# Performance work log

Hardware: AMD Instinct MI355X
Metric: run time of the kernel (lower is better)

## Reference

```python
import jax, jax.numpy as jnp
import numpy as np

N_NODES = 100000
N_EDGES = 1600000
T = 24
F_IN = 16
H = 128
OUT = 64


def setup_inputs() -> dict:
    key = jax.random.key(0)
    ks = jax.random.split(key, 12)
    s = 0.05
    return {
        "x_time_series": jax.random.normal(ks[0], (N_NODES, T, F_IN), jnp.float32),
        "edge_index": jax.random.randint(ks[1], (2, N_EDGES), 0, N_NODES, jnp.int64),
        "gru_W_ih": jax.random.normal(ks[2], (3 * H, F_IN), jnp.float32) * s,
        "gru_W_hh": jax.random.normal(ks[3], (3 * H, H), jnp.float32) * s,
        "gru_b_ih": jax.random.normal(ks[4], (3 * H,), jnp.float32) * s,
        "gru_b_hh": jax.random.normal(ks[5], (3 * H,), jnp.float32) * s,
        "lin1_l_W": jax.random.normal(ks[6], (H, H), jnp.float32) * s,
        "lin1_l_b": jax.random.normal(ks[7], (H,), jnp.float32) * s,
        "lin1_r_W": jax.random.normal(ks[8], (H, H), jnp.float32) * s,
        "lin2_l_W": jax.random.normal(ks[9], (OUT, H), jnp.float32) * s,
        "lin2_l_b": jax.random.normal(ks[10], (OUT,), jnp.float32) * s,
        "lin2_r_W": jax.random.normal(ks[11], (OUT, H), jnp.float32) * s,
    }


def gru_last(x, W_ih, W_hh, b_ih, b_hh):
    # x: [N, T, F]; single-layer batch_first GRU, return last hidden state [N, H]
    Hd = W_hh.shape[1]
    # precompute input projections for all steps: [T, N, 3H]
    gi_all = jnp.einsum('ntf,gf->tng', x, W_ih) + b_ih

    def step(h, gi):
        gh = h @ W_hh.T + b_hh
        r = jax.nn.sigmoid(gi[:, :Hd] + gh[:, :Hd])
        z = jax.nn.sigmoid(gi[:, Hd:2 * Hd] + gh[:, Hd:2 * Hd])
        n = jnp.tanh(gi[:, 2 * Hd:] + r * gh[:, 2 * Hd:])
        h_new = (1.0 - z) * n + z * h
        return h_new, None

    h0 = jnp.zeros((x.shape[0], Hd), x.dtype)
    h_last, _ = jax.lax.scan(step, h0, gi_all)
    return h_last


def sage_conv(x, edge_index, W_l, b_l, W_r):
    # PyG SAGEConv with mean aggregation:
    #   out_i = W_l @ mean_{j->i} x_j + b_l + W_r @ x_i
    src, dst = edge_index[0], edge_index[1]
    n = x.shape[0]
    msg = x[src]                                   # [E, F] irregular gather
    agg = jax.ops.segment_sum(msg, dst, num_segments=n)
    cnt = jax.ops.segment_sum(jnp.ones((msg.shape[0],), x.dtype), dst, num_segments=n)
    mean = agg / jnp.maximum(cnt, 1.0)[:, None]
    return mean @ W_l.T + b_l + x @ W_r.T


def reference(x_time_series, edge_index, gru_W_ih, gru_W_hh, gru_b_ih, gru_b_hh,
              lin1_l_W, lin1_l_b, lin1_r_W, lin2_l_W, lin2_l_b, lin2_r_W):
    x = x_time_series.reshape(-1, T, F_IN)
    h = gru_last(x, gru_W_ih, gru_W_hh, gru_b_ih, gru_b_hh)   # [N, H]
    g = sage_conv(h, edge_index, lin1_l_W, lin1_l_b, lin1_r_W) + h
    g = jax.nn.relu(g)
    # dropout in eval mode -> identity
    out = sage_conv(g, edge_index, lin2_l_W, lin2_l_b, lin2_r_W)
    return out
```

## Files before the change

### kernel.cpp

```cpp
#include <hip/hip_runtime.h>
#include <math.h>

#define NND 100000
#define TT 24
#define FI 16
#define HD 128
#define GD 384
#define OD 64
#define NE 1600000

typedef __bf16 bf16x8 __attribute__((ext_vector_type(8)));
typedef float f32x4 __attribute__((ext_vector_type(4)));
typedef unsigned short u16;
typedef unsigned int u32;

#define S_RZ (-1.44269504f)
#define S_N  (-2.88539008f)

__device__ __forceinline__ u16 f2b(float f) {
    u32 u = __float_as_uint(f);
    u32 r = (u + 0x7FFFu + ((u >> 16) & 1u)) >> 16;
    return (u16)r;
}
__device__ __forceinline__ u32 cvtpk(float lo, float hi) {
    u32 r;
    asm("v_cvt_pk_bf16_f32 %0, %1, %2" : "=v"(r) : "v"(lo), "v"(hi));
    return r;
}
__device__ __forceinline__ float b2f(u16 v) {
    return __uint_as_float((u32)v << 16);
}

__global__ void cvt_x_kernel(const float* __restrict__ x, u16* __restrict__ xb) {
    size_t base = ((size_t)blockIdx.x * 256 + threadIdx.x) * 8;
    float4 a = *(const float4*)(x + base);
    float4 b = *(const float4*)(x + base + 4);
    u32 o0 = cvtpk(a.x, a.y), o1 = cvtpk(a.z, a.w);
    u32 o2 = cvtpk(b.x, b.y), o3 = cvtpk(b.z, b.w);
    *(uint4*)(xb + base) = make_uint4(o0, o1, o2, o3);
}

__global__ void pack_w_kernel(const float* __restrict__ Whh, const float* __restrict__ Wih,
                              const float* __restrict__ bih, const float* __restrict__ bhh,
                              u16* __restrict__ Ap, u16* __restrict__ Aip) {
    int id = blockIdx.x * 256 + threadIdx.x;
    if (id < 6144) {
        int lane = id & 63, fs = id >> 6;
        int s = fs & 3, gt = fs >> 2;
        int row = gt * 16 + (lane & 15);
        float sc = (row < 2 * HD) ? S_RZ : S_N;
        int k0 = s * 32 + (lane >> 4) * 8;
        const float* src = Whh + (size_t)row * HD + k0;
        u16 o[8];
#pragma unroll
        for (int e = 0; e < 8; ++e) o[e] = f2b(src[e] * sc);
        u32* dst = (u32*)(Ap + (size_t)id * 8);
#pragma unroll
        for (int e = 0; e < 4; ++e) dst[e] = (u32)o[2 * e] | ((u32)o[2 * e + 1] << 16);
    } else if (id < 7680) {
        int id2 = id - 6144;
        int lane = id2 & 63, gt = id2 >> 6;
        int row = gt * 16 + (lane & 15);
        float sc = (row < 2 * HD) ? S_RZ : S_N;
        int g = lane >> 4;
        u16 o[8] = {0, 0, 0, 0, 0, 0, 0, 0};
        if (g < 2) {
            const float* src = Wih + (size_t)row * FI + g * 8;
#pragma unroll
            for (int e = 0; e < 8; ++e) o[e] = f2b(src[e] * sc);
        } else if (g == 2) {
            float bias = (row < 2 * HD) ? (bih[row] + bhh[row]) : bih[row];
            o[0] = f2b(bias * sc);
        }
        u32* dst = (u32*)(Aip + (size_t)id2 * 8);
#pragma unroll
        for (int e = 0; e < 4; ++e) dst[e] = (u32)o[2 * e] | ((u32)o[2 * e + 1] << 16);
    }
}

__global__ void pack_gemm_kernel(const float* __restrict__ W, u16* __restrict__ F, int rows) {
    int id = blockIdx.x * 256 + threadIdx.x;
    if (id >= rows * 16) return;
    int lane = id & 63, fs = id >> 6;
    int s = fs & 3, tile = fs >> 2;
    int row = tile * 16 + (lane & 15);
    int k0 = s * 32 + (lane >> 4) * 8;
    const float* src = W + (size_t)row * HD + k0;
    u16 o[8];
#pragma unroll
    for (int e = 0; e < 8; ++e) o[e] = f2b(src[e]);
    u32* dst = (u32*)(F + (size_t)id * 8);
#pragma unroll
    for (int e = 0; e < 4; ++e) dst[e] = (u32)o[2 * e] | ((u32)o[2 * e + 1] << 16);
}

__device__ __forceinline__ int hidx(int row, int col) {
    return row * 128 + (col ^ ((row & 7) << 3));
}

__global__ __launch_bounds__(512) void gru_mfma_kernel(
    const u16* __restrict__ xb,
    const u16* __restrict__ Ap,
    const u16* __restrict__ Aip,
    const float* __restrict__ bhh,
    float* __restrict__ hout,
    u16* __restrict__ h16)
{
    __shared__ u16 hb0[64 * 128];
    __shared__ u16 hb1[64 * 128];

    const int tid = threadIdx.x;
    const int w = tid >> 6, lane = tid & 63;
    const int l15 = lane & 15, g = lane >> 4;
    const int gbase = blockIdx.x * 64;
    const int j0 = w * 16 + g * 4;

    for (int i = tid; i < 64 * 128 / 2; i += 512) ((u32*)hb0)[i] = 0u;

    bf16x8 Ah[3][4], Ai[3];
#pragma unroll
    for (int a = 0; a < 3; ++a) {
        int gt = w + a * 8;
#pragma unroll
        for (int s = 0; s < 4; ++s)
            Ah[a][s] = *(const bf16x8*)(Ap + ((size_t)(gt * 4 + s) * 64 + lane) * 8);
        Ai[a] = *(const bf16x8*)(Aip + ((size_t)gt * 64 + lane) * 8);
    }

    f32x4 bnh4 = *(const f32x4*)(bhh + 256 + j0);
#pragma unroll
    for (int r = 0; r < 4; ++r) bnh4[r] *= S_N;

    const f32x4 fz = {0.f, 0.f, 0.f, 0.f};
    bf16x8 xdef;
    {
        uint4 u = make_uint4(0u, 0u, 0u, 0u);
        if (g == 2) u.x = 0x3F80u;
        *(uint4*)&xdef = u;
    }

    f32x4 hreg[4];
#pragma unroll
    for (int m = 0; m < 4; ++m) hreg[m] = fz;

    int xoff[4];
#pragma unroll
    for (int m = 0; m < 4; ++m) {
        int nd = gbase + m * 16 + l15;
        nd = nd < NND ? nd : NND - 1;
        xoff[m] = nd * (TT * FI) + g * 8;
    }

    __syncthreads();

    auto dostep = [&](int t, const u16* __restrict__ rb, u16* __restrict__ wb) {
#pragma unroll
        for (int mh = 0; mh < 2; ++mh) {
            const int ma = mh * 2, mb = mh * 2 + 1;
            bf16x8 xf0 = xdef, xf1 = xdef;
            if (g < 2) {
                xf0 = *(const bf16x8*)(xb + (size_t)(xoff[ma] + t * FI));
                xf1 = *(const bf16x8*)(xb + (size_t)(xoff[mb] + t * FI));
            }

            const int ra = ma * 16 + l15, rbr = mb * 16 + l15;
            bf16x8 b0[4], b1[4];
#pragma unroll
            for (int s = 0; s < 4; ++s) {
                b0[s] = *(const bf16x8*)&rb[hidx(ra, s * 32 + g * 8)];
                b1[s] = *(const bf16x8*)&rb[hidx(rbr, s * 32 + g * 8)];
            }

            f32x4 acc[3][2], acci[2];
#pragma unroll
            for (int a = 0; a < 3; ++a) {
                acc[a][0] = __builtin_amdgcn_mfma_f32_16x16x32_bf16(Ah[a][0], b0[0], fz, 0, 0, 0);
                acc[a][1] = __builtin_amdgcn_mfma_f32_16x16x32_bf16(Ah[a][0], b1[0], fz, 0, 0, 0);
            }
#pragma unroll
            for (int s = 1; s < 4; ++s) {
#pragma unroll
                for (int a = 0; a < 3; ++a) {
                    acc[a][0] = __builtin_amdgcn_mfma_f32_16x16x32_bf16(Ah[a][s], b0[s], acc[a][0], 0, 0, 0);
                    acc[a][1] = __builtin_amdgcn_mfma_f32_16x16x32_bf16(Ah[a][s], b1[s], acc[a][1], 0, 0, 0);
                }
            }
            acc[0][0] = __builtin_amdgcn_mfma_f32_16x16x32_bf16(Ai[0], xf0, acc[0][0], 0, 0, 0);
            acc[1][0] = __builtin_amdgcn_mfma_f32_16x16x32_bf16(Ai[1], xf0, acc[1][0], 0, 0, 0);
            acci[0]   = __builtin_amdgcn_mfma_f32_16x16x32_bf16(Ai[2], xf0, fz, 0, 0, 0);
            acc[0][1] = __builtin_amdgcn_mfma_f32_16x16x32_bf16(Ai[0], xf1, acc[0][1], 0, 0, 0);
            acc[1][1] = __builtin_amdgcn_mfma_f32_16x16x32_bf16(Ai[1], xf1, acc[1][1], 0, 0, 0);
            acci[1]   = __builtin_amdgcn_mfma_f32_16x16x32_bf16(Ai[2], xf1, fz, 0, 0, 0);

#pragma unroll
            for (int mi = 0; mi < 2; ++mi) {
                int m = mh * 2 + mi;
#pragma unroll
                for (int r = 0; r < 4; ++r) {
                    float rr = __builtin_amdgcn_rcpf(1.0f + __builtin_amdgcn_exp2f(acc[0][mi][r]));
                    float zz = __builtin_amdgcn_rcpf(1.0f + __builtin_amdgcn_exp2f(acc[1][mi][r]));
                    float na = acci[mi][r] + rr * (acc[2][mi][r] + bnh4[r]);
                    float nn = 2.0f * __builtin_amdgcn_rcpf(1.0f + __builtin_amdgcn_exp2f(na)) - 1.0f;
                    float h = nn + zz * (hreg[m][r] - nn);
                    hreg[m][r] = h;
                }
                u32 p0 = cvtpk(hreg[m][0], hreg[m][1]);
                u32 p1 = cvtpk(hreg[m][2], hreg[m][3]);
                *(uint2*)&wb[hidx(m * 16 + l15, j0)] = make_uint2(p0, p1);
            }
        }
        __syncthreads();
    };

#pragma unroll 1
    for (int tt = 0; tt < TT; tt += 2) {
        dostep(tt, hb0, hb1);
        dostep(tt + 1, hb1, hb0);
    }

#pragma unroll
    for (int m = 0; m < 4; ++m) {
        int nd = gbase + m * 16 + l15;
        if (nd < NND) {
            *(f32x4*)(hout + (size_t)nd * HD + j0) = hreg[m];
            u32 c0 = cvtpk(hreg[m][0], hreg[m][1]);
            u32 c1 = cvtpk(hreg[m][2], hreg[m][3]);
            *(uint2*)(h16 + (size_t)nd * HD + j0) = make_uint2(c0, c1);
        }
    }
}

template <int M, bool RES>
__global__ __launch_bounds__(512) void proj2_mfma_kernel(
    const u16* __restrict__ X16,
    const u16* __restrict__ Wl,
    const u16* __restrict__ Wr,
    const float* __restrict__ bias,
    const float* __restrict__ Xres,
    u16* __restrict__ P16,
    float* __restrict__ Q)
{
    __shared__ u16 xs[64 * 128];

    const int tid = threadIdx.x;
    const int w = tid >> 6, lane = tid & 63;
    const int l15 = lane & 15, g = lane >> 4;
    const int gbase = blockIdx.x * 64;
    const f32x4 fz = {0.f, 0.f, 0.f, 0.f};

#pragma unroll
    for (int i = 0; i < 2; ++i) {
        int lin = tid + 512 * i;
        int n = lin >> 4;
        int k8 = (lin & 15) * 8;
        int gn = gbase + n; if (gn >= NND) gn = NND - 1;
        uint4 v = *(const uint4*)(X16 + (size_t)gn * HD + k8);
        *(uint4*)&xs[hidx(n, k8)] = v;
    }
    __syncthreads();

    if constexpr (M == 128) {
        bf16x8 Al[4], Ar[4];
#pragma unroll
        for (int s = 0; s < 4; ++s) {
            Al[s] = *(const bf16x8*)(Wl + ((size_t)(w * 4 + s) * 64 + lane) * 8);
            Ar[s] = *(const bf16x8*)(Wr + ((size_t)(w * 4 + s) * 64 + lane) * 8);
        }
        const int f0 = w * 16 + g * 4;
        f32x4 bq = *(const f32x4*)(bias + f0);

#pragma unroll
        for (int m = 0; m < 4; ++m) {
            bf16x8 b[4];
#pragma unroll
            for (int s = 0; s < 4; ++s)
                b[s] = *(const bf16x8*)&xs[hidx(m * 16 + l15, s * 32 + g * 8)];
            f32x4 ap = fz, aq = fz;
#pragma unroll
            for (int s = 0; s < 4; ++s) {
                ap = __builtin_amdgcn_mfma_f32_16x16x32_bf16(Al[s], b[s], ap, 0, 0, 0);
                aq = __builtin_amdgcn_mfma_f32_16x16x32_bf16(Ar[s], b[s], aq, 0, 0, 0);
            }
            int nd = gbase + m * 16 + l15;
            if (nd < NND) {
                u32 c0 = cvtpk(ap[0], ap[1]), c1 = cvtpk(ap[2], ap[3]);
                *(uint2*)(P16 + (size_t)nd * M + f0) = make_uint2(c0, c1);
                f32x4 v = aq + bq;
                if constexpr (RES) v += *(const f32x4*)(Xres + (size_t)nd * HD + f0);
                *(f32x4*)(Q + (size_t)nd * M + f0) = v;
            }
        }
    } else {
        const int tile = w & 3;
        const bool isQ = (w >= 4);
        const u16* Wsel = isQ ? Wr : Wl;
        bf16x8 A[4];
#pragma unroll
        for (int s = 0; s < 4; ++s)
            A[s] = *(const bf16x8*)(Wsel + ((size_t)(tile * 4 + s) * 64 + lane) * 8);
        const int f0 = tile * 16 + g * 4;
        f32x4 bq = *(const f32x4*)(bias + f0);

#pragma unroll
        for (int m = 0; m < 4; ++m) {
            bf16x8 b[4];
#pragma unroll
            for (int s = 0; s < 4; ++s)
                b[s] = *(const bf16x8*)&xs[hidx(m * 16 + l15, s * 32 + g * 8)];
            f32x4 a = fz;
#pragma unroll
            for (int s = 0; s < 4; ++s)
                a = __builtin_amdgcn_mfma_f32_16x16x32_bf16(A[s], b[s], a, 0, 0, 0);
            int nd = gbase + m * 16 + l15;
            if (nd < NND) {
                if (isQ) {
                    f32x4 v = a + bq;
                    *(f32x4*)(Q + (size_t)nd * M + f0) = v;
                } else {
                    u32 c0 = cvtpk(a[0], a[1]), c1 = cvtpk(a[2], a[3]);
                    *(uint2*)(P16 + (size_t)nd * M + f0) = make_uint2(c0, c1);
                }
            }
        }
    }
}

__global__ void count_kernel(const int* __restrict__ dst, int* __restrict__ cnt) {
    int e = blockIdx.x * 256 + threadIdx.x;
    if (e < NE) atomicAdd(&cnt[dst[e]], 1);
}

__global__ void blocksum_kernel(const int* __restrict__ cnt, int* __restrict__ bsum) {
    __shared__ int sh[256];
    int b = blockIdx.x, t = threadIdx.x;
    int base = b * 1024;
    int s = 0;
    for (int i = t; i < 1024; i += 256) {
        int idx = base + i;
        s += (idx < NND) ? cnt[idx] : 0;
    }
    sh[t] = s; __syncthreads();
    for (int o = 128; o > 0; o >>= 1) { if (t < o) sh[t] += sh[t + o]; __syncthreads(); }
    if (t == 0) bsum[b] = sh[0];
}

__global__ void scanbsum_kernel(int* __restrict__ bsum, int nb, int* __restrict__ rowptr) {
    if (threadIdx.x == 0 && blockIdx.x == 0) {
        int acc = 0;
        for (int i = 0; i < nb; ++i) { int v = bsum[i]; bsum[i] = acc; acc += v; }
        rowptr[NND] = NE;
    }
}

__global__ void scan_kernel(const int* __restrict__ cnt, const int* __restrict__ bsum,
                            int* __restrict__ rowptr) {
    __shared__ int sh[256];
    int b = blockIdx.x, t = threadIdx.x;
    int base = b * 1024;
    int v[4], loc = 0;
#pragma unroll
    for (int j = 0; j < 4; ++j) {
        int idx = base + t * 4 + j;
        v[j] = (idx < NND) ? cnt[idx] : 0;
        loc += v[j];
    }
    sh[t] = loc; __syncthreads();
    for (int o = 1; o < 256; o <<= 1) {
        int x = (t >= o) ? sh[t - o] : 0;
        __syncthreads();
        sh[t] += x;
        __syncthreads();
    }
    int acc = bsum[b] + sh[t] - loc;
#pragma unroll
    for (int j = 0; j < 4; ++j) {
        int idx = base + t * 4 + j;
        if (idx < NND) rowptr[idx] = acc;
        acc += v[j];
    }
}

__global__ void fill_kernel(const int* __restrict__ src, const int* __restrict__ dst,
                            const int* __restrict__ rowptr, int* __restrict__ fill,
                            int* __restrict__ csr) {
    int e = blockIdx.x * 256 + threadIdx.x;
    if (e >= NE) return;
    int d = dst[e];
    int pos = rowptr[d] + atomicAdd(&fill[d], 1);
    csr[pos] = src[e];
}

__global__ __launch_bounds__(256) void gather1_kernel(
    const u16* __restrict__ P16,
    const int* __restrict__ rowptr, const int* __restrict__ csr,
    const float* __restrict__ q,
    u16* __restrict__ g16)
{
    int n = ((blockIdx.x * 256 + threadIdx.x) >> 6);
    if (n >= NND) return;
    int lane = threadIdx.x & 63;
    int beg = rowptr[n], end = rowptr[n + 1];

    float ax = 0.f, ay = 0.f;
    for (int cb = beg; cb < end; cb += 64) {
        int myi = (cb + lane < end) ? csr[cb + lane] : 0;
        int nn = min(end - cb, 64);
        for (int i = 0; i < nn; ++i) {
            int s = __shfl(myi, i);
            u32 pv = *(const u32*)(P16 + (size_t)s * HD + lane * 2);
            ax += b2f((u16)pv); ay += b2f((u16)(pv >> 16));
        }
    }
    int deg = end - beg;
    float inv = 1.0f / (float)(deg > 0 ? deg : 1);
    float2 qv = *(const float2*)(q + (size_t)n * HD + lane * 2);
    float r0 = fmaxf(ax * inv + qv.x, 0.f);
    float r1 = fmaxf(ay * inv + qv.y, 0.f);
    *(u32*)(g16 + (size_t)n * HD + lane * 2) = cvtpk(r0, r1);
}

__global__ __launch_bounds__(256) void gather2_kernel(
    const u16* __restrict__ P16,
    const int* __restrict__ rowptr, const int* __restrict__ csr,
    const float* __restrict__ q,
    float* __restrict__ outp)
{
    int n = ((blockIdx.x * 256 + threadIdx.x) >> 6);
    if (n >= NND) return;
    int lane = threadIdx.x & 63;
    int beg = rowptr[n], end = rowptr[n + 1];

    float a = 0.f;
    for (int cb = beg; cb < end; cb += 64) {
        int myi = (cb + lane < end) ? csr[cb + lane] : 0;
        int nn = min(end - cb, 64);
        for (int i = 0; i < nn; ++i) {
            int s = __shfl(myi, i);
            a += b2f(P16[(size_t)s * OD + lane]);
        }
    }
    int deg = end - beg;
    float inv = 1.0f / (float)(deg > 0 ? deg : 1);
    outp[(size_t)n * OD + lane] = a * inv + q[(size_t)n * OD + lane];
}

extern "C" void kernel_launch(void* const* d_in, const int* in_sizes, int n_in,
                              void* d_out, int out_size, void* d_ws, size_t ws_size,
                              hipStream_t stream) {
    const float* x   = (const float*)d_in[0];
    const int*   edg = (const int*)d_in[1];
    const int*   src = edg;
    const int*   dst = edg + NE;
    const float* Wih = (const float*)d_in[2];
    const float* Whh = (const float*)d_in[3];
    const float* bih = (const float*)d_in[4];
    const float* bhh = (const float*)d_in[5];
    const float* W1l = (const float*)d_in[6];
    const float* b1  = (const float*)d_in[7];
    const float* W1r = (const float*)d_in[8];
    const float* W2l = (const float*)d_in[9];
    const float* b2  = (const float*)d_in[10];
    const float* W2r = (const float*)d_in[11];
    float* out = (float*)d_out;

    char* wsp = (char*)d_ws;
    auto alloc = [&](size_t nbytes) {
        char* p = wsp; wsp += (nbytes + 255) & ~(size_t)255; return p;
    };
    u16*   Ap    = (u16*)alloc((size_t)6144 * 8 * 2);
    u16*   Aip   = (u16*)alloc((size_t)1536 * 8 * 2);
    u16*   Pw1l  = (u16*)alloc((size_t)2048 * 8 * 2);
    u16*   Pw1r  = (u16*)alloc((size_t)2048 * 8 * 2);
    u16*   Pw2l  = (u16*)alloc((size_t)1024 * 8 * 2);
    u16*   Pw2r  = (u16*)alloc((size_t)1024 * 8 * 2);
    int*   cnt   = (int*)alloc((size_t)NND * 4);
    int*   fill  = (int*)alloc((size_t)NND * 4);
    int*   rowp  = (int*)alloc((size_t)(NND + 1) * 4);
    int*   bsum  = (int*)alloc((size_t)128 * 4);
    int*   csr   = (int*)alloc((size_t)NE * 4);
    float* h     = (float*)alloc((size_t)NND * HD * 4);
    u16*   h16   = (u16*)alloc((size_t)NND * HD * 2);
    float* q     = (float*)alloc((size_t)NND * HD * 4);
    u16*   P16   = (u16*)alloc((size_t)NND * HD * 2);
    u16*   g16   = (u16*)alloc((size_t)NND * HD * 2);
    u16*   xb    = (u16*)q;
    float* q2    = q;
    u16*   P16b  = P16;

    const int NB_SCAN = (NND + 1023) / 1024;

    hipMemsetAsync(cnt, 0, (size_t)NND * 4, stream);
    hipMemsetAsync(fill, 0, (size_t)NND * 4, stream);

    cvt_x_kernel<<<(NND * TT * FI) / (256 * 8), 256, 0, stream>>>(x, xb);
    pack_w_kernel<<<30, 256, 0, stream>>>(Whh, Wih, bih, bhh, Ap, Aip);
    pack_gemm_kernel<<<8, 256, 0, stream>>>(W1l, Pw1l, HD);
    pack_gemm_kernel<<<8, 256, 0, stream>>>(W1r, Pw1r, HD);
    pack_gemm_kernel<<<4, 256, 0, stream>>>(W2l, Pw2l, OD);
    pack_gemm_kernel<<<4, 256, 0, stream>>>(W2r, Pw2r, OD);

    count_kernel<<<(NE + 255) / 256, 256, 0, stream>>>(dst, cnt);
    blocksum_kernel<<<NB_SCAN, 256, 0, stream>>>(cnt, bsum);
    scanbsum_kernel<<<1, 64, 0, stream>>>(bsum, NB_SCAN, rowp);
    scan_kernel<<<NB_SCAN, 256, 0, stream>>>(cnt, bsum, rowp);
    fill_kernel<<<(NE + 255) / 256, 256, 0, stream>>>(src, dst, rowp, fill, csr);

    const int nblk = (NND + 63) / 64;
    gru_mfma_kernel<<<nblk, 512, 0, stream>>>(xb, Ap, Aip, bhh, h, h16);

    proj2_mfma_kernel<HD, true><<<nblk, 512, 0, stream>>>(h16, Pw1l, Pw1r, b1, h, P16, q);
    gather1_kernel<<<(NND * 64 + 255) / 256, 256, 0, stream>>>(P16, rowp, csr, q, g16);

    proj2_mfma_kernel<OD, false><<<nblk, 512, 0, stream>>>(g16, Pw2l, Pw2r, b2, nullptr, P16b, q2);
    gather2_kernel<<<(NND * 64 + 255) / 256, 256, 0, stream>>>(P16b, rowp, csr, q2, out);
}
```

Before: 850.2 us.

## Fuse layer-1 projections into GRU epilogue and layer-2 projection into gather

```diff
diff --git a/kernel.cpp b/kernel.cpp
--- a/kernel.cpp
+++ b/kernel.cpp
@@ -103,8 +103,11 @@
     const u16* __restrict__ Ap,
     const u16* __restrict__ Aip,
     const float* __restrict__ bhh,
-    float* __restrict__ hout,
-    u16* __restrict__ h16)
+    const u16* __restrict__ Wl,
+    const u16* __restrict__ Wr,
+    const float* __restrict__ b1,
+    u16* __restrict__ P16,
+    float* __restrict__ q)
 {
     __shared__ u16 hb0[64 * 128];
     __shared__ u16 hb1[64 * 128];
@@ -164,25 +167,25 @@
             }
 
             const int ra = ma * 16 + l15, rbr = mb * 16 + l15;
-            bf16x8 b0[4], b1[4];
+            bf16x8 b0[4], b1f[4];
 #pragma unroll
             for (int s = 0; s < 4; ++s) {
-                b0[s] = *(const bf16x8*)&rb[hidx(ra, s * 32 + g * 8)];
-                b1[s] = *(const bf16x8*)&rb[hidx(rbr, s * 32 + g * 8)];
+                b0[s]  = *(const bf16x8*)&rb[hidx(ra, s * 32 + g * 8)];
+                b1f[s] = *(const bf16x8*)&rb[hidx(rbr, s * 32 + g * 8)];
             }
 
             f32x4 acc[3][2], acci[2];
 #pragma unroll
             for (int a = 0; a < 3; ++a) {
                 acc[a][0] = __builtin_amdgcn_mfma_f32_16x16x32_bf16(Ah[a][0], b0[0], fz, 0, 0, 0);
-                acc[a][1] = __builtin_amdgcn_mfma_f32_16x16x32_bf16(Ah[a][0], b1[0], fz, 0, 0, 0);
+                acc[a][1] = __builtin_amdgcn_mfma_f32_16x16x32_bf16(Ah[a][0], b1f[0], fz, 0, 0, 0);
             }
 #pragma unroll
             for (int s = 1; s < 4; ++s) {
 #pragma unroll
                 for (int a = 0; a < 3; ++a) {
                     acc[a][0] = __builtin_amdgcn_mfma_f32_16x16x32_bf16(Ah[a][s], b0[s], acc[a][0], 0, 0, 0);
-                    acc[a][1] = __builtin_amdgcn_mfma_f32_16x16x32_bf16(Ah[a][s], b1[s], acc[a][1], 0, 0, 0);
+                    acc[a][1] = __builtin_amdgcn_mfma_f32_16x16x32_bf16(Ah[a][s], b1f[s], acc[a][1], 0, 0, 0);
                 }
             }
             acc[0][0] = __builtin_amdgcn_mfma_f32_16x16x32_bf16(Ai[0], xf0, acc[0][0], 0, 0, 0);
@@ -218,109 +221,32 @@
         dostep(tt + 1, hb1, hb0);
     }
 
+    bf16x8 Al[4], Ar[4];
+#pragma unroll
+    for (int s = 0; s < 4; ++s) {
+        Al[s] = *(const bf16x8*)(Wl + ((size_t)(w * 4 + s) * 64 + lane) * 8);
+        Ar[s] = *(const bf16x8*)(Wr + ((size_t)(w * 4 + s) * 64 + lane) * 8);
+    }
+    f32x4 bq = *(const f32x4*)(b1 + j0);
+
 #pragma unroll
     for (int m = 0; m < 4; ++m) {
+        bf16x8 b[4];
+#pragma unroll
+        for (int s = 0; s < 4; ++s)
+            b[s] = *(const bf16x8*)&hb0[hidx(m * 16 + l15, s * 32 + g * 8)];
+        f32x4 ap = fz, aq = fz;
+#pragma unroll
+        for (int s = 0; s < 4; ++s) {
+            ap = __builtin_amdgcn_mfma_f32_16x16x32_bf16(Al[s], b[s], ap, 0, 0, 0);
+            aq = __builtin_amdgcn_mfma_f32_16x16x32_bf16(Ar[s], b[s], aq, 0, 0, 0);
+        }
         int nd = gbase + m * 16 + l15;
         if (nd < NND) {
-            *(f32x4*)(hout + (size_t)nd * HD + j0) = hreg[m];
-            u32 c0 = cvtpk(hreg[m][0], hreg[m][1]);
-            u32 c1 = cvtpk(hreg[m][2], hreg[m][3]);
-            *(uint2*)(h16 + (size_t)nd * HD + j0) = make_uint2(c0, c1);
-        }
-    }
-}
-
-template <int M, bool RES>
-__global__ __launch_bounds__(512) void proj2_mfma_kernel(
-    const u16* __restrict__ X16,
-    const u16* __restrict__ Wl,
-    const u16* __restrict__ Wr,
-    const float* __restrict__ bias,
-    const float* __restrict__ Xres,
-    u16* __restrict__ P16,
-    float* __restrict__ Q)
-{
-    __shared__ u16 xs[64 * 128];
-
-    const int tid = threadIdx.x;
-    const int w = tid >> 6, lane = tid & 63;
-    const int l15 = lane & 15, g = lane >> 4;
-    const int gbase = blockIdx.x * 64;
-    const f32x4 fz = {0.f, 0.f, 0.f, 0.f};
-
-#pragma unroll
-    for (int i = 0; i < 2; ++i) {
-        int lin = tid + 512 * i;
-        int n = lin >> 4;
-        int k8 = (lin & 15) * 8;
-        int gn = gbase + n; if (gn >= NND) gn = NND - 1;
-        uint4 v = *(const uint4*)(X16 + (size_t)gn * HD + k8);
-        *(uint4*)&xs[hidx(n, k8)] = v;
-    }
-    __syncthreads();
-
-    if constexpr (M == 128) {
-        bf16x8 Al[4], Ar[4];
-#pragma unroll
-        for (int s = 0; s < 4; ++s) {
-            Al[s] = *(const bf16x8*)(Wl + ((size_t)(w * 4 + s) * 64 + lane) * 8);
-            Ar[s] = *(const bf16x8*)(Wr + ((size_t)(w * 4 + s) * 64 + lane) * 8);
-        }
-        const int f0 = w * 16 + g * 4;
-        f32x4 bq = *(const f32x4*)(bias + f0);
-
-#pragma unroll
-        for (int m = 0; m < 4; ++m) {
-            bf16x8 b[4];
-#pragma unroll
-            for (int s = 0; s < 4; ++s)
-                b[s] = *(const bf16x8*)&xs[hidx(m * 16 + l15, s * 32 + g * 8)];
-            f32x4 ap = fz, aq = fz;
-#pragma unroll
-            for (int s = 0; s < 4; ++s) {
-                ap = __builtin_amdgcn_mfma_f32_16x16x32_bf16(Al[s], b[s], ap, 0, 0, 0);
-                aq = __builtin_amdgcn_mfma_f32_16x16x32_bf16(Ar[s], b[s], aq, 0, 0, 0);
-            }
-            int nd = gbase + m * 16 + l15;
-            if (nd < NND) {
-                u32 c0 = cvtpk(ap[0], ap[1]), c1 = cvtpk(ap[2], ap[3]);
-                *(uint2*)(P16 + (size_t)nd * M + f0) = make_uint2(c0, c1);
-                f32x4 v = aq + bq;
-                if constexpr (RES) v += *(const f32x4*)(Xres + (size_t)nd * HD + f0);
-                *(f32x4*)(Q + (size_t)nd * M + f0) = v;
-            }
-        }
-    } else {
-        const int tile = w & 3;
-        const bool isQ = (w >= 4);
-        const u16* Wsel = isQ ? Wr : Wl;
-        bf16x8 A[4];
-#pragma unroll
-        for (int s = 0; s < 4; ++s)
-            A[s] = *(const bf16x8*)(Wsel + ((size_t)(tile * 4 + s) * 64 + lane) * 8);
-        const int f0 = tile * 16 + g * 4;
-        f32x4 bq = *(const f32x4*)(bias + f0);
-
-#pragma unroll
-        for (int m = 0; m < 4; ++m) {
-            bf16x8 b[4];
-#pragma unroll
-            for (int s = 0; s < 4; ++s)
-                b[s] = *(const bf16x8*)&xs[hidx(m * 16 + l15, s * 32 + g * 8)];
-            f32x4 a = fz;
-#pragma unroll
-            for (int s = 0; s < 4; ++s)
-                a = __builtin_amdgcn_mfma_f32_16x16x32_bf16(A[s], b[s], a, 0, 0, 0);
-            int nd = gbase + m * 16 + l15;
-            if (nd < NND) {
-                if (isQ) {
-                    f32x4 v = a + bq;
-                    *(f32x4*)(Q + (size_t)nd * M + f0) = v;
-                } else {
-                    u32 c0 = cvtpk(a[0], a[1]), c1 = cvtpk(a[2], a[3]);
-                    *(uint2*)(P16 + (size_t)nd * M + f0) = make_uint2(c0, c1);
-                }
-            }
+            u32 c0 = cvtpk(ap[0], ap[1]), c1 = cvtpk(ap[2], ap[3]);
+            *(uint2*)(P16 + (size_t)nd * HD + j0) = make_uint2(c0, c1);
+            f32x4 v = aq + bq + hreg[m];
+            *(f32x4*)(q + (size_t)nd * HD + j0) = v;
         }
     }
 }
@@ -390,39 +316,86 @@
     csr[pos] = src[e];
 }
 
-__global__ __launch_bounds__(256) void gather1_kernel(
+__global__ __launch_bounds__(512) void gather_proj_kernel(
     const u16* __restrict__ P16,
     const int* __restrict__ rowptr, const int* __restrict__ csr,
     const float* __restrict__ q,
-    u16* __restrict__ g16)
+    const u16* __restrict__ W2l, const u16* __restrict__ W2r,
+    const float* __restrict__ b2,
+    u16* __restrict__ P2,
+    float* __restrict__ q2)
 {
-    int n = ((blockIdx.x * 256 + threadIdx.x) >> 6);
-    if (n >= NND) return;
-    int lane = threadIdx.x & 63;
-    int beg = rowptr[n], end = rowptr[n + 1];
-
-    float ax = 0.f, ay = 0.f;
-    for (int cb = beg; cb < end; cb += 64) {
-        int myi = (cb + lane < end) ? csr[cb + lane] : 0;
-        int nn = min(end - cb, 64);
-        for (int i = 0; i < nn; ++i) {
-            int s = __shfl(myi, i);
-            u32 pv = *(const u32*)(P16 + (size_t)s * HD + lane * 2);
-            ax += b2f((u16)pv); ay += b2f((u16)(pv >> 16));
-        }
-    }
-    int deg = end - beg;
-    float inv = 1.0f / (float)(deg > 0 ? deg : 1);
-    float2 qv = *(const float2*)(q + (size_t)n * HD + lane * 2);
-    float r0 = fmaxf(ax * inv + qv.x, 0.f);
-    float r1 = fmaxf(ay * inv + qv.y, 0.f);
-    *(u32*)(g16 + (size_t)n * HD + lane * 2) = cvtpk(r0, r1);
+    __shared__ u16 xs[64 * 128];
+
+    const int tid = threadIdx.x;
+    const int w = tid >> 6, lane = tid & 63;
+    const int l15 = lane & 15, g = lane >> 4;
+    const int gbase = blockIdx.x * 64;
+    const f32x4 fz = {0.f, 0.f, 0.f, 0.f};
+
+#pragma unroll 1
+    for (int i = 0; i < 8; ++i) {
+        int nloc = w * 8 + i;
+        int n = gbase + nloc;
+        u32 gv = 0u;
+        if (n < NND) {
+            int beg = rowptr[n], end = rowptr[n + 1];
+            float ax = 0.f, ay = 0.f;
+            for (int cb = beg; cb < end; cb += 64) {
+                int myi = (cb + lane < end) ? csr[cb + lane] : 0;
+                int nn = min(end - cb, 64);
+                for (int ii = 0; ii < nn; ++ii) {
+                    int s = __shfl(myi, ii);
+                    u32 pv = *(const u32*)(P16 + (size_t)s * HD + lane * 2);
+                    ax += b2f((u16)pv); ay += b2f((u16)(pv >> 16));
+                }
+            }
+            int deg = end - beg;
+            float inv = 1.0f / (float)(deg > 0 ? deg : 1);
+            float2 qv = *(const float2*)(q + (size_t)n * HD + lane * 2);
+            gv = cvtpk(fmaxf(ax * inv + qv.x, 0.f), fmaxf(ay * inv + qv.y, 0.f));
+        }
+        *(u32*)&xs[hidx(nloc, lane * 2)] = gv;
+    }
+    __syncthreads();
+
+    const int tile = w & 3;
+    const bool isQ = (w >= 4);
+    const u16* Wsel = isQ ? W2r : W2l;
+    bf16x8 A[4];
+#pragma unroll
+    for (int s = 0; s < 4; ++s)
+        A[s] = *(const bf16x8*)(Wsel + ((size_t)(tile * 4 + s) * 64 + lane) * 8);
+    const int f0 = tile * 16 + g * 4;
+    f32x4 bq = *(const f32x4*)(b2 + f0);
+
+#pragma unroll
+    for (int m = 0; m < 4; ++m) {
+        bf16x8 b[4];
+#pragma unroll
+        for (int s = 0; s < 4; ++s)
+            b[s] = *(const bf16x8*)&xs[hidx(m * 16 + l15, s * 32 + g * 8)];
+        f32x4 a = fz;
+#pragma unroll
+        for (int s = 0; s < 4; ++s)
+            a = __builtin_amdgcn_mfma_f32_16x16x32_bf16(A[s], b[s], a, 0, 0, 0);
+        int nd = gbase + m * 16 + l15;
+        if (nd < NND) {
+            if (isQ) {
+                f32x4 v = a + bq;
+                *(f32x4*)(q2 + (size_t)nd * OD + f0) = v;
+            } else {
+                u32 c0 = cvtpk(a[0], a[1]), c1 = cvtpk(a[2], a[3]);
+                *(uint2*)(P2 + (size_t)nd * OD + f0) = make_uint2(c0, c1);
+            }
+        }
+    }
 }
 
 __global__ __launch_bounds__(256) void gather2_kernel(
-    const u16* __restrict__ P16,
+    const u16* __restrict__ P2,
     const int* __restrict__ rowptr, const int* __restrict__ csr,
-    const float* __restrict__ q,
+    const float* __restrict__ q2,
     float* __restrict__ outp)
 {
     int n = ((blockIdx.x * 256 + threadIdx.x) >> 6);
@@ -436,12 +409,12 @@
         int nn = min(end - cb, 64);
         for (int i = 0; i < nn; ++i) {
             int s = __shfl(myi, i);
-            a += b2f(P16[(size_t)s * OD + lane]);
+            a += b2f(P2[(size_t)s * OD + lane]);
         }
     }
     int deg = end - beg;
     float inv = 1.0f / (float)(deg > 0 ? deg : 1);
-    outp[(size_t)n * OD + lane] = a * inv + q[(size_t)n * OD + lane];
+    outp[(size_t)n * OD + lane] = a * inv + q2[(size_t)n * OD + lane];
 }
 
 extern "C" void kernel_launch(void* const* d_in, const int* in_sizes, int n_in,
@@ -478,14 +451,11 @@
     int*   rowp  = (int*)alloc((size_t)(NND + 1) * 4);
     int*   bsum  = (int*)alloc((size_t)128 * 4);
     int*   csr   = (int*)alloc((size_t)NE * 4);
-    float* h     = (float*)alloc((size_t)NND * HD * 4);
-    u16*   h16   = (u16*)alloc((size_t)NND * HD * 2);
+    u16*   xb    = (u16*)alloc((size_t)NND * TT * FI * 2);
     float* q     = (float*)alloc((size_t)NND * HD * 4);
     u16*   P16   = (u16*)alloc((size_t)NND * HD * 2);
-    u16*   g16   = (u16*)alloc((size_t)NND * HD * 2);
-    u16*   xb    = (u16*)q;
-    float* q2    = q;
-    u16*   P16b  = P16;
+    u16*   P2    = (u16*)alloc((size_t)NND * OD * 2);
+    float* q2    = (float*)alloc((size_t)NND * OD * 4);
 
     const int NB_SCAN = (NND + 1023) / 1024;
 
@@ -506,11 +476,9 @@
     fill_kernel<<<(NE + 255) / 256, 256, 0, stream>>>(src, dst, rowp, fill, csr);
 
     const int nblk = (NND + 63) / 64;
-    gru_mfma_kernel<<<nblk, 512, 0, stream>>>(xb, Ap, Aip, bhh, h, h16);
-
-    proj2_mfma_kernel<HD, true><<<nblk, 512, 0, stream>>>(h16, Pw1l, Pw1r, b1, h, P16, q);
-    gather1_kernel<<<(NND * 64 + 255) / 256, 256, 0, stream>>>(P16, rowp, csr, q, g16);
-
-    proj2_mfma_kernel<OD, false><<<nblk, 512, 0, stream>>>(g16, Pw2l, Pw2r, b2, nullptr, P16b, q2);
-    gather2_kernel<<<(NND * 64 + 255) / 256, 256, 0, stream>>>(P16b, rowp, csr, q2, out);
-}
+    gru_mfma_kernel<<<nblk, 512, 0, stream>>>(xb, Ap, Aip, bhh, Pw1l, Pw1r, b1, P16, q);
+
+    gather_proj_kernel<<<nblk, 512, 0, stream>>>(P16, rowp, csr, q, Pw2l, Pw2r, b2, P2, q2);
+
+    gather2_kernel<<<(NND * 64 + 255) / 256, 256, 0, stream>>>(P2, rowp, csr, q2, out);
+}
```

Result: faster. 831.9 us (-2.2%).
